# Optimization experiments

Hardware: AMD Instinct MI355X
Metric: run time of the kernel (lower is better)

The kernel has to match this reference:

```python
import jax, jax.numpy as jnp
import numpy as np


def setup_inputs() -> dict:
    key = jax.random.key(0)
    ks = jax.random.split(key, 9)
    B, C, H, W = 16, 64, 64, 64
    s = 0.02
    return {
        "x": jax.random.normal(ks[0], (B, C, H, W), dtype=jnp.float32),
        "qw": jax.random.normal(ks[1], (C, C), dtype=jnp.float32) * s,
        "qb": jax.random.normal(ks[2], (C,), dtype=jnp.float32) * s,
        "kw": jax.random.normal(ks[3], (C, C), dtype=jnp.float32) * s,
        "kb": jax.random.normal(ks[4], (C,), dtype=jnp.float32) * s,
        "vw": jax.random.normal(ks[5], (C, C), dtype=jnp.float32) * s,
        "vb": jax.random.normal(ks[6], (C,), dtype=jnp.float32) * s,
        "ow": jax.random.normal(ks[7], (C, C), dtype=jnp.float32) * s,
        "ob": jax.random.normal(ks[8], (C,), dtype=jnp.float32) * s,
    }


def reference(x, qw, qb, kw, kb, vw, vb, ow, ob):
    # x: [B, C, H, W]; 1x1 convs == per-pixel linear maps with weight [out_ch, in_ch]
    B, C, H, W = x.shape
    S = H * W
    xt = x.reshape(B, C, S).transpose(0, 2, 1)  # [B, S, C] tokens over spatial positions
    Q = jnp.einsum("bsc,oc->bso", xt, qw) + qb
    K = jnp.einsum("bsc,oc->bso", xt, kw) + kb
    V = jnp.einsum("bsc,oc->bso", xt, vw) + vb
    scale = 1.0 / jnp.sqrt(jnp.asarray(C, dtype=x.dtype))
    scores = jnp.einsum("bqc,bkc->bqk", Q, K) * scale  # [B, S, S]
    attn = jax.nn.softmax(scores, axis=-1)
    out = jnp.einsum("bqk,bkc->bqc", attn, V)  # [B, S, C]
    out = jnp.einsum("bsc,oc->bso", out, ow) + ob  # out 1x1 conv
    return out.transpose(0, 2, 1).reshape(B, C, H, W)
```

## Files before the change

kernel.cpp:

```cpp
#include <hip/hip_runtime.h>
#include <stdint.h>

#define SS 4096
#define CC 64
#define BB 16

typedef unsigned short u16;
typedef __attribute__((ext_vector_type(8))) __bf16 bf16x8;
typedef __attribute__((ext_vector_type(8))) short short8;
typedef __attribute__((ext_vector_type(4))) float f32x4;

__device__ __forceinline__ uint32_t pkbf(float a, float b) {
    uint32_t ua = __float_as_uint(a) + 0x8000u;
    uint32_t ub = __float_as_uint(b) + 0x8000u;
    return __builtin_amdgcn_perm(ub, ua, 0x07060302u);
}

__device__ __forceinline__ bf16x8 ldw8(const float* p) {
    f32x4 lo = *(const f32x4*)(p);
    f32x4 hi = *(const f32x4*)(p + 4);
    union { uint32_t u[4]; bf16x8 v; } r;
    r.u[0] = pkbf(lo[0], lo[1]);
    r.u[1] = pkbf(lo[2], lo[3]);
    r.u[2] = pkbf(hi[0], hi[1]);
    r.u[3] = pkbf(hi[2], hi[3]);
    return r.v;
}

__global__ __launch_bounds__(256, 4) void qkv_kernel(
    const float* __restrict__ x,
    const float* __restrict__ qw, const float* __restrict__ qb,
    const float* __restrict__ kw, const float* __restrict__ kb,
    const float* __restrict__ vw, const float* __restrict__ vb,
    u16* __restrict__ Q, u16* __restrict__ K, u16* __restrict__ VT)
{
    const int b    = blockIdx.x & 15;
    const int s0   = (blockIdx.x >> 4) << 6;
    const int tid  = threadIdx.x;
    const int w    = tid >> 6;
    const int lane = tid & 63;
    const int lq   = lane & 15;
    const int quad = lane >> 4;

    __shared__ u16 wt[3][64 * 72];
    __shared__ u16 xt[64 * 72];

    for (int m = 0; m < 3; ++m) {
        const float* wsrc = (m == 0) ? qw : ((m == 1) ? kw : vw);
#pragma unroll
        for (int i = 0; i < 8; ++i) {
            int p  = tid + (i << 8);
            int o  = p >> 5;
            int cp = p & 31;
            const float* wp = wsrc + o * 64 + cp * 2;
            ((uint32_t*)&wt[m][o * 72])[cp] = pkbf(wp[0], wp[1]);
        }
    }
    {
        const int sl = tid & 63;
        const int g  = tid >> 6;
        const float* xp = x + (size_t)b * CC * SS + s0 + sl;
#pragma unroll
        for (int i = 0; i < 8; ++i) {
            int p = g + (i << 2);
            float f0 = xp[(size_t)(2 * p) * SS];
            float f1 = xp[(size_t)(2 * p + 1) * SS];
            ((uint32_t*)&xt[sl * 72])[p] = pkbf(f0, f1);
        }
    }
    __syncthreads();

    bf16x8 a0 = *(const bf16x8*)&xt[(w * 16 + lq) * 72 + quad * 8];
    bf16x8 a1 = *(const bf16x8*)&xt[(w * 16 + lq) * 72 + 32 + quad * 8];
    __syncthreads();

    u16* bb = xt + w * (16 * 72);

    const float QSCALE = 0.125f * 1.44269504088896340736f;

    for (int m = 0; m < 3; ++m) {
        const float* bsrc = (m == 0) ? qb : ((m == 1) ? kb : vb);
        bf16x8 bfr[2][4];
#pragma unroll
        for (int kc = 0; kc < 2; ++kc)
#pragma unroll
            for (int nt = 0; nt < 4; ++nt)
                bfr[kc][nt] = *(const bf16x8*)&wt[m][(nt * 16 + lq) * 72 + kc * 32 + quad * 8];

        f32x4 acc[4];
#pragma unroll
        for (int nt = 0; nt < 4; ++nt) {
            float bv = bsrc[nt * 16 + lq];
            acc[nt] = (f32x4){bv, bv, bv, bv};
        }
#pragma unroll
        for (int nt = 0; nt < 4; ++nt) {
            acc[nt] = __builtin_amdgcn_mfma_f32_16x16x32_bf16(a0, bfr[0][nt], acc[nt], 0, 0, 0);
            acc[nt] = __builtin_amdgcn_mfma_f32_16x16x32_bf16(a1, bfr[1][nt], acc[nt], 0, 0, 0);
        }

        if (m == 2) {
#pragma unroll
            for (int nt = 0; nt < 4; ++nt) {
                int c = nt * 16 + lq;
                uint2 pv;
                pv.x = pkbf(acc[nt][0], acc[nt][1]);
                pv.y = pkbf(acc[nt][2], acc[nt][3]);
                *(uint2*)(VT + ((size_t)(b * CC + c)) * SS + s0 + w * 16 + quad * 4) = pv;
            }
        } else {
            const float scl = (m == 0) ? QSCALE : 1.0f;
#pragma unroll
            for (int nt = 0; nt < 4; ++nt)
#pragma unroll
                for (int r = 0; r < 4; ++r)
                    bb[(quad * 4 + r) * 72 + nt * 16 + lq] =
                        (u16)((__float_as_uint(acc[nt][r] * scl) + 0x8000u) >> 16);

            const int row = lane >> 2;
            const int ch  = (lane & 3) << 4;
            short8 v0 = *(const short8*)&bb[row * 72 + ch];
            short8 v1 = *(const short8*)&bb[row * 72 + ch + 8];
            u16* dst = ((m == 0) ? Q : K) + ((size_t)(b * SS + s0 + w * 16 + row)) * CC + ch;
            *(short8*)dst = v0;
            *(short8*)(dst + 8) = v1;
        }
    }
}

__global__ __launch_bounds__(256, 2) void flash_kernel(
    const u16* __restrict__ Q, const u16* __restrict__ K,
    const u16* __restrict__ Vt, const float* __restrict__ ow,
    const float* __restrict__ ob, float* __restrict__ out)
{
    const int b    = blockIdx.x & 15;
    const int q0   = (blockIdx.x >> 4) << 7;
    const int tid  = threadIdx.x;
    const int w    = tid >> 6;
    const int lane = tid & 63;
    const int lq   = lane & 15;
    const int quad = lane >> 4;

    __shared__ u16 lds_k[2][64 * 64];
    __shared__ u16 lds_v[2][64 * 64];
    __shared__ u16 lds_p[8][16 * 64];

    bf16x8 qf[2][2];
#pragma unroll
    for (int g = 0; g < 2; ++g) {
        const u16* qp = Q + ((size_t)(b * SS + q0 + g * 64 + w * 16 + lq)) * CC + quad * 8;
        qf[g][0] = *(const bf16x8*)(qp);
        qf[g][1] = *(const bf16x8*)(qp + 32);
    }

    f32x4 ot[2][4];
#pragma unroll
    for (int g = 0; g < 2; ++g)
#pragma unroll
        for (int ct = 0; ct < 4; ++ct) ot[g][ct] = (f32x4){0.f, 0.f, 0.f, 0.f};
    float lp[2][4] = {{0.f, 0.f, 0.f, 0.f}, {0.f, 0.f, 0.f, 0.f}};

    const int srow = tid >> 2;
    const int a    = tid & 3;
    const u16* kg = K + ((size_t)(b * SS + srow)) * CC + a * 16;
    const u16* vg = Vt + ((size_t)(b * CC + srow)) * SS + a * 16;
    const int sw0 = srow * 64 + (((a << 1)    ) ^ (srow & 7)) * 8;
    const int sw1 = srow * 64 + (((a << 1) | 1) ^ (srow & 7)) * 8;

    {
        short8 k0 = *(const short8*)(kg);
        short8 k1 = *(const short8*)(kg + 8);
        short8 v0 = *(const short8*)(vg);
        short8 v1 = *(const short8*)(vg + 8);
        *(short8*)&lds_k[0][sw0] = k0;
        *(short8*)&lds_k[0][sw1] = k1;
        *(short8*)&lds_v[0][sw0] = v0;
        *(short8*)&lds_v[0][sw1] = v1;
    }

    const int lsw = lq & 7;
    u16* pw0 = lds_p[(w << 1)];
    u16* pw1 = lds_p[(w << 1) | 1];

    for (int kt = 0; kt < 64; ++kt) {
        __syncthreads();
        const int buf = kt & 1;

        const int ktn = (kt + 1) & 63;
        const u16* kgn = kg + (size_t)ktn * (64 * CC);
        const u16* vgn = vg + ktn * 64;
        short8 nk0 = *(const short8*)(kgn);
        short8 nk1 = *(const short8*)(kgn + 8);
        short8 nv0 = *(const short8*)(vgn);
        short8 nv1 = *(const short8*)(vgn + 8);

        bf16x8 kf[2][4];
#pragma unroll
        for (int kc = 0; kc < 2; ++kc)
#pragma unroll
            for (int mt = 0; mt < 4; ++mt)
                kf[kc][mt] = *(const bf16x8*)
                    &lds_k[buf][(mt * 16 + lq) * 64 + (((kc << 2) + quad) ^ lsw) * 8];

        f32x4 sa[2][4];
#pragma unroll
        for (int g = 0; g < 2; ++g)
#pragma unroll
            for (int mt = 0; mt < 4; ++mt) sa[g][mt] = (f32x4){0.f, 0.f, 0.f, 0.f};
#pragma unroll
        for (int g = 0; g < 2; ++g)
#pragma unroll
            for (int kc = 0; kc < 2; ++kc)
#pragma unroll
                for (int mt = 0; mt < 4; ++mt)
                    sa[g][mt] = __builtin_amdgcn_mfma_f32_16x16x32_bf16(
                        kf[kc][mt], qf[g][kc], sa[g][mt], 0, 0, 0);

#pragma unroll
        for (int g = 0; g < 2; ++g) {
            u16* pw = g ? pw1 : pw0;
#pragma unroll
            for (int mt = 0; mt < 4; ++mt) {
                float p0 = __builtin_amdgcn_exp2f(sa[g][mt][0]);
                float p1 = __builtin_amdgcn_exp2f(sa[g][mt][1]);
                float p2 = __builtin_amdgcn_exp2f(sa[g][mt][2]);
                float p3 = __builtin_amdgcn_exp2f(sa[g][mt][3]);
                lp[g][0] += p0; lp[g][1] += p1; lp[g][2] += p2; lp[g][3] += p3;
                uint2 pv;
                pv.x = pkbf(p0, p1);
                pv.y = pkbf(p2, p3);
                *(uint2*)&pw[lq * 64 + (((mt * 2 + (quad >> 1)) ^ lsw) << 3) + (quad & 1) * 4] = pv;
            }
        }

        bf16x8 vf[2][4];
#pragma unroll
        for (int kc = 0; kc < 2; ++kc)
#pragma unroll
            for (int ct = 0; ct < 4; ++ct)
                vf[kc][ct] = *(const bf16x8*)
                    &lds_v[buf][(ct * 16 + lq) * 64 + (((kc << 2) + quad) ^ lsw) * 8];

#pragma unroll
        for (int g = 0; g < 2; ++g) {
            const u16* pw = g ? pw1 : pw0;
#pragma unroll
            for (int kc = 0; kc < 2; ++kc) {
                bf16x8 pf = *(const bf16x8*)
                    &pw[lq * 64 + (((kc * 4 + quad) ^ lsw) << 3)];
#pragma unroll
                for (int ct = 0; ct < 4; ++ct)
                    ot[g][ct] = __builtin_amdgcn_mfma_f32_16x16x32_bf16(
                        vf[kc][ct], pf, ot[g][ct], 0, 0, 0);
            }
        }

        u16* lkd = lds_k[buf ^ 1];
        u16* lvd = lds_v[buf ^ 1];
        *(short8*)&lkd[sw0] = nk0;
        *(short8*)&lkd[sw1] = nk1;
        *(short8*)&lvd[sw0] = nv0;
        *(short8*)&lvd[sw1] = nv1;
    }

    bf16x8 wf[2][4];
#pragma unroll
    for (int kc = 0; kc < 2; ++kc)
#pragma unroll
        for (int nt = 0; nt < 4; ++nt)
            wf[kc][nt] = ldw8(ow + (nt * 16 + lq) * 64 + kc * 32 + quad * 8);
    float bias[4];
#pragma unroll
    for (int nt = 0; nt < 4; ++nt) bias[nt] = ob[nt * 16 + lq];

#pragma unroll
    for (int g = 0; g < 2; ++g) {
        float l = (lp[g][0] + lp[g][1]) + (lp[g][2] + lp[g][3]);
        l += __shfl_xor(l, 16);
        l += __shfl_xor(l, 32);
        const float inv = 1.0f / l;

        u16* po = g ? pw1 : pw0;
#pragma unroll
        for (int ct = 0; ct < 4; ++ct) {
            uint2 pv;
            pv.x = pkbf(ot[g][ct][0] * inv, ot[g][ct][1] * inv);
            pv.y = pkbf(ot[g][ct][2] * inv, ot[g][ct][3] * inv);
            *(uint2*)&po[lq * 64 + (((ct * 2 + (quad >> 1)) ^ lsw) << 3) + (quad & 1) * 4] = pv;
        }
        bf16x8 oa0 = *(const bf16x8*)&po[lq * 64 + (((0 * 4 + quad) ^ lsw) << 3)];
        bf16x8 oa1 = *(const bf16x8*)&po[lq * 64 + (((1 * 4 + quad) ^ lsw) << 3)];

        f32x4 acc[4];
#pragma unroll
        for (int nt = 0; nt < 4; ++nt)
            acc[nt] = (f32x4){bias[nt], bias[nt], bias[nt], bias[nt]};
#pragma unroll
        for (int nt = 0; nt < 4; ++nt) {
            acc[nt] = __builtin_amdgcn_mfma_f32_16x16x32_bf16(oa0, wf[0][nt], acc[nt], 0, 0, 0);
            acc[nt] = __builtin_amdgcn_mfma_f32_16x16x32_bf16(oa1, wf[1][nt], acc[nt], 0, 0, 0);
        }
#pragma unroll
        for (int nt = 0; nt < 4; ++nt) {
            float* dst = out + ((size_t)(b * CC + nt * 16 + lq)) * SS
                       + q0 + g * 64 + w * 16 + quad * 4;
            *(f32x4*)dst = acc[nt];
        }
    }
}

extern "C" void kernel_launch(void* const* d_in, const int* in_sizes, int n_in,
                              void* d_out, int out_size, void* d_ws, size_t ws_size,
                              hipStream_t stream)
{
    const float* x  = (const float*)d_in[0];
    const float* qw = (const float*)d_in[1];
    const float* qb = (const float*)d_in[2];
    const float* kw = (const float*)d_in[3];
    const float* kb = (const float*)d_in[4];
    const float* vw = (const float*)d_in[5];
    const float* vb = (const float*)d_in[6];
    const float* ow = (const float*)d_in[7];
    const float* ob = (const float*)d_in[8];
    float* out = (float*)d_out;

    const size_t T = (size_t)BB * SS * CC;
    u16* Q  = (u16*)d_ws;
    u16* K  = Q + T;
    u16* VT = K + T;

    qkv_kernel<<<dim3(BB * 64), dim3(256), 0, stream>>>(x, qw, qb, kw, kb, vw, vb, Q, K, VT);
    flash_kernel<<<dim3(BB * 32), dim3(256), 0, stream>>>(Q, K, VT, ow, ob, out);
}
```

Before: 182.0 us.

## Keep softmax probabilities in registers by permuting V layout in LDS

The P tile no longer round-trips through LDS. The exp2 outputs, already in the MFMA accumulator layout, are packed directly into bf16x8 B operands for the PV MFMA. To match the reordered k index, V rows are stored to LDS as 4-element pieces in a permuted swizzled layout. s_setprio is also raised around the MFMA blocks so this wave keeps priority during matrix work. This removes the LDS writes and reads of P per tile, at the cost of more, smaller LDS stores for V and possible bank conflicts.

```diff
diff --git a/kernel.cpp b/kernel.cpp
--- a/kernel.cpp
+++ b/kernel.cpp
@@ -8,6 +8,7 @@
 typedef unsigned short u16;
 typedef __attribute__((ext_vector_type(8))) __bf16 bf16x8;
 typedef __attribute__((ext_vector_type(8))) short short8;
+typedef __attribute__((ext_vector_type(4))) short s16x4;
 typedef __attribute__((ext_vector_type(4))) float f32x4;
 
 __device__ __forceinline__ uint32_t pkbf(float a, float b) {
@@ -164,18 +165,28 @@
     const int a    = tid & 3;
     const u16* kg = K + ((size_t)(b * SS + srow)) * CC + a * 16;
     const u16* vg = Vt + ((size_t)(b * CC + srow)) * SS + a * 16;
-    const int sw0 = srow * 64 + (((a << 1)    ) ^ (srow & 7)) * 8;
-    const int sw1 = srow * 64 + (((a << 1) | 1) ^ (srow & 7)) * 8;
+    const int ssw = srow & 7;
+    const int sw0 = srow * 64 + ((((a << 1)    ) ^ ssw) << 3);
+    const int sw1 = srow * 64 + ((((a << 1) | 1) ^ ssw) << 3);
+    const int kcs = (a >> 1) << 2;
+    const int us  = (a & 1) << 2;
+    const int vw0 = srow * 64 + (((kcs + 0) ^ ssw) << 3) + us;
+    const int vw1 = srow * 64 + (((kcs + 1) ^ ssw) << 3) + us;
+    const int vw2 = srow * 64 + (((kcs + 2) ^ ssw) << 3) + us;
+    const int vw3 = srow * 64 + (((kcs + 3) ^ ssw) << 3) + us;
 
     {
         short8 k0 = *(const short8*)(kg);
         short8 k1 = *(const short8*)(kg + 8);
-        short8 v0 = *(const short8*)(vg);
-        short8 v1 = *(const short8*)(vg + 8);
+        union { short8 v; s16x4 h[2]; } v0, v1;
+        v0.v = *(const short8*)(vg);
+        v1.v = *(const short8*)(vg + 8);
         *(short8*)&lds_k[0][sw0] = k0;
         *(short8*)&lds_k[0][sw1] = k1;
-        *(short8*)&lds_v[0][sw0] = v0;
-        *(short8*)&lds_v[0][sw1] = v1;
+        *(s16x4*)&lds_v[0][vw0] = v0.h[0];
+        *(s16x4*)&lds_v[0][vw1] = v0.h[1];
+        *(s16x4*)&lds_v[0][vw2] = v1.h[0];
+        *(s16x4*)&lds_v[0][vw3] = v1.h[1];
     }
 
     const int lsw = lq & 7;
@@ -191,8 +202,9 @@
         const u16* vgn = vg + ktn * 64;
         short8 nk0 = *(const short8*)(kgn);
         short8 nk1 = *(const short8*)(kgn + 8);
-        short8 nv0 = *(const short8*)(vgn);
-        short8 nv1 = *(const short8*)(vgn + 8);
+        union { short8 v; s16x4 h[2]; } nv0, nv1;
+        nv0.v = *(const short8*)(vgn);
+        nv1.v = *(const short8*)(vgn + 8);
 
         bf16x8 kf[2][4];
 #pragma unroll
@@ -207,6 +219,7 @@
         for (int g = 0; g < 2; ++g)
 #pragma unroll
             for (int mt = 0; mt < 4; ++mt) sa[g][mt] = (f32x4){0.f, 0.f, 0.f, 0.f};
+        __builtin_amdgcn_s_setprio(1);
 #pragma unroll
         for (int g = 0; g < 2; ++g)
 #pragma unroll
@@ -215,10 +228,19 @@
                 for (int mt = 0; mt < 4; ++mt)
                     sa[g][mt] = __builtin_amdgcn_mfma_f32_16x16x32_bf16(
                         kf[kc][mt], qf[g][kc], sa[g][mt], 0, 0, 0);
+        __builtin_amdgcn_s_setprio(0);
+
+        bf16x8 vf[2][4];
+#pragma unroll
+        for (int kc = 0; kc < 2; ++kc)
+#pragma unroll
+            for (int ct = 0; ct < 4; ++ct)
+                vf[kc][ct] = *(const bf16x8*)
+                    &lds_v[buf][(ct * 16 + lq) * 64 + (((kc << 2) + quad) ^ lsw) * 8];
 
 #pragma unroll
         for (int g = 0; g < 2; ++g) {
-            u16* pw = g ? pw1 : pw0;
+            union { uint32_t u[4]; bf16x8 v; } pf[2];
 #pragma unroll
             for (int mt = 0; mt < 4; ++mt) {
                 float p0 = __builtin_amdgcn_exp2f(sa[g][mt][0]);
@@ -226,41 +248,27 @@
                 float p2 = __builtin_amdgcn_exp2f(sa[g][mt][2]);
                 float p3 = __builtin_amdgcn_exp2f(sa[g][mt][3]);
                 lp[g][0] += p0; lp[g][1] += p1; lp[g][2] += p2; lp[g][3] += p3;
-                uint2 pv;
-                pv.x = pkbf(p0, p1);
-                pv.y = pkbf(p2, p3);
-                *(uint2*)&pw[lq * 64 + (((mt * 2 + (quad >> 1)) ^ lsw) << 3) + (quad & 1) * 4] = pv;
+                pf[mt >> 1].u[(mt & 1) * 2 + 0] = pkbf(p0, p1);
+                pf[mt >> 1].u[(mt & 1) * 2 + 1] = pkbf(p2, p3);
             }
-        }
-
-        bf16x8 vf[2][4];
-#pragma unroll
-        for (int kc = 0; kc < 2; ++kc)
-#pragma unroll
-            for (int ct = 0; ct < 4; ++ct)
-                vf[kc][ct] = *(const bf16x8*)
-                    &lds_v[buf][(ct * 16 + lq) * 64 + (((kc << 2) + quad) ^ lsw) * 8];
-
-#pragma unroll
-        for (int g = 0; g < 2; ++g) {
-            const u16* pw = g ? pw1 : pw0;
-#pragma unroll
-            for (int kc = 0; kc < 2; ++kc) {
-                bf16x8 pf = *(const bf16x8*)
-                    &pw[lq * 64 + (((kc * 4 + quad) ^ lsw) << 3)];
+            __builtin_amdgcn_s_setprio(1);
+#pragma unroll
+            for (int kc = 0; kc < 2; ++kc)
 #pragma unroll
                 for (int ct = 0; ct < 4; ++ct)
                     ot[g][ct] = __builtin_amdgcn_mfma_f32_16x16x32_bf16(
-                        vf[kc][ct], pf, ot[g][ct], 0, 0, 0);
-            }
+                        vf[kc][ct], pf[kc].v, ot[g][ct], 0, 0, 0);
+            __builtin_amdgcn_s_setprio(0);
         }
 
         u16* lkd = lds_k[buf ^ 1];
         u16* lvd = lds_v[buf ^ 1];
         *(short8*)&lkd[sw0] = nk0;
         *(short8*)&lkd[sw1] = nk1;
-        *(short8*)&lvd[sw0] = nv0;
-        *(short8*)&lvd[sw1] = nv1;
+        *(s16x4*)&lvd[vw0] = nv0.h[0];
+        *(s16x4*)&lvd[vw1] = nv0.h[1];
+        *(s16x4*)&lvd[vw2] = nv1.h[0];
+        *(s16x4*)&lvd[vw3] = nv1.h[1];
     }
 
     bf16x8 wf[2][4];
```

Measured after the change: 168.8 us. 7.3% less time.
